# Performance work log

Hardware: AMD Instinct MI355X
Metric: run time of the kernel (lower is better)

Reference implementation:

```python
import jax, jax.numpy as jnp
import numpy as np

D_MODEL = 2048
D_INNER = 4096  # d_model * expand_factor
LN_EPS = 1e-5


def setup_inputs() -> dict:
    key = jax.random.key(0)
    k1, k2, k3, k4 = jax.random.split(key, 4)
    B, S = 2, 4096
    x = jax.random.normal(k1, (B, S, D_MODEL), dtype=jnp.float32)
    gamma = jnp.ones((D_MODEL,), dtype=jnp.float32)
    beta = jnp.zeros((D_MODEL,), dtype=jnp.float32)
    # nn.Linear-like small init to keep activations in-range
    W_in = jax.random.normal(k2, (2 * D_INNER, D_MODEL), dtype=jnp.float32) * 0.02
    W_out = jax.random.normal(k3, (D_MODEL, D_INNER), dtype=jnp.float32) * 0.02
    dt_min, dt_max = 0.001, 0.1
    dt = jax.random.uniform(k4, (D_INNER,), dtype=jnp.float32) * (dt_max - dt_min) + dt_min
    return {"x": x, "gamma": gamma, "beta": beta, "W_in": W_in, "W_out": W_out, "dt": dt}


def reference(x, gamma, beta, W_in, W_out, dt):
    # x: [B, S, D_MODEL]
    identity = x
    # LayerNorm over last dim
    mu = jnp.mean(x, axis=-1, keepdims=True)
    var = jnp.mean(jnp.square(x - mu), axis=-1, keepdims=True)
    xn = (x - mu) * jax.lax.rsqrt(var + LN_EPS) * gamma + beta
    # in_proj: [B, S, 2*D_INNER]
    projected = jnp.einsum("bsd,ed->bse", xn, W_in)
    z, gate = jnp.split(projected, 2, axis=-1)
    # z gated by sigmoid of clamped z (clamp only inside sigmoid)
    z_gated = z * jax.nn.sigmoid(jnp.clip(z, -15.0, 15.0))
    # temporal weighting by softmax(-dt) over d_inner
    dt_weights = jax.nn.softmax(-dt)  # [D_INNER]
    z_temporal = z_gated * dt_weights  # broadcast over [B, S, D_INNER]
    # gate path: silu on clamped gate
    output = z_temporal * jax.nn.silu(jnp.clip(gate, -15.0, 15.0))
    # out_proj back to d_model
    output = jnp.einsum("bse,de->bsd", output, W_out)
    return output + identity
```

## Files before the change

kernel.cpp:

```cpp
#include <hip/hip_runtime.h>
#include <cstdint>
#include <cstddef>

#define T_TOK 8192
#define DM    2048
#define DI    4096
#define TWO_DI 8192

typedef __attribute__((ext_vector_type(8))) short bf16x8;
typedef __attribute__((ext_vector_type(4))) float f32x4;

__device__ __forceinline__ unsigned short f2bf(float f) {
  union { float f; unsigned u; } c; c.f = f;
  unsigned u = c.u;
  unsigned r = (u + 0x7fffu + ((u >> 16) & 1u)) >> 16;
  return (unsigned short)r;
}

__global__ __launch_bounds__(256) void ln_kernel(
    const float* __restrict__ x, const float* __restrict__ gamma,
    const float* __restrict__ beta, unsigned short* __restrict__ xn) {
  const int t = blockIdx.x;
  const int tid = threadIdx.x;
  const float* row = x + (size_t)t * DM;
  float4 v0 = reinterpret_cast<const float4*>(row)[tid];
  float4 v1 = reinterpret_cast<const float4*>(row)[tid + 256];
  float s  = v0.x + v0.y + v0.z + v0.w + v1.x + v1.y + v1.z + v1.w;
  float ss = v0.x*v0.x + v0.y*v0.y + v0.z*v0.z + v0.w*v0.w
           + v1.x*v1.x + v1.y*v1.y + v1.z*v1.z + v1.w*v1.w;
  #pragma unroll
  for (int off = 32; off > 0; off >>= 1) {
    s  += __shfl_down(s, off);
    ss += __shfl_down(ss, off);
  }
  __shared__ float red[8];
  __shared__ float mu_s, inv_s;
  if ((tid & 63) == 0) { red[tid >> 6] = s; red[4 + (tid >> 6)] = ss; }
  __syncthreads();
  if (tid == 0) {
    float S  = red[0] + red[1] + red[2] + red[3];
    float SS = red[4] + red[5] + red[6] + red[7];
    float mu  = S * (1.0f / DM);
    float var = SS * (1.0f / DM) - mu * mu;
    mu_s = mu;
    inv_s = rsqrtf(var + 1e-5f);
  }
  __syncthreads();
  const float mu = mu_s, inv = inv_s;
  float4 g0 = reinterpret_cast<const float4*>(gamma)[tid];
  float4 b0 = reinterpret_cast<const float4*>(beta)[tid];
  float4 g1 = reinterpret_cast<const float4*>(gamma)[tid + 256];
  float4 b1 = reinterpret_cast<const float4*>(beta)[tid + 256];
  ushort4 o0, o1;
  o0.x = f2bf((v0.x - mu) * inv * g0.x + b0.x);
  o0.y = f2bf((v0.y - mu) * inv * g0.y + b0.y);
  o0.z = f2bf((v0.z - mu) * inv * g0.z + b0.z);
  o0.w = f2bf((v0.w - mu) * inv * g0.w + b0.w);
  o1.x = f2bf((v1.x - mu) * inv * g1.x + b1.x);
  o1.y = f2bf((v1.y - mu) * inv * g1.y + b1.y);
  o1.z = f2bf((v1.z - mu) * inv * g1.z + b1.z);
  o1.w = f2bf((v1.w - mu) * inv * g1.w + b1.w);
  reinterpret_cast<ushort4*>(xn + (size_t)t * DM)[tid]       = o0;
  reinterpret_cast<ushort4*>(xn + (size_t)t * DM)[tid + 256] = o1;
}

__global__ __launch_bounds__(256) void cvt_both(
    const float* __restrict__ a, unsigned short* __restrict__ oa, int n4a,
    const float* __restrict__ b, unsigned short* __restrict__ ob, int n4b) {
  int i = blockIdx.x * 256 + threadIdx.x;
  const float* src;
  unsigned short* dst;
  int idx;
  if (i < n4a) { src = a; dst = oa; idx = i; }
  else { idx = i - n4a; if (idx >= n4b) return; src = b; dst = ob; }
  float4 v = reinterpret_cast<const float4*>(src)[idx];
  ushort4 o;
  o.x = f2bf(v.x); o.y = f2bf(v.y); o.z = f2bf(v.z); o.w = f2bf(v.w);
  reinterpret_cast<ushort4*>(dst)[idx] = o;
}

__global__ __launch_bounds__(256) void dt_softmax(
    const float* __restrict__ dt, float* __restrict__ w) {
  const int tid = threadIdx.x;
  float e[16];
  float local = 0.f;
  #pragma unroll
  for (int i = 0; i < 16; ++i) {
    float v = __expf(-dt[i * 256 + tid]);
    e[i] = v;
    local += v;
  }
  #pragma unroll
  for (int off = 32; off > 0; off >>= 1) local += __shfl_down(local, off);
  __shared__ float red[4];
  __shared__ float tot;
  if ((tid & 63) == 0) red[tid >> 6] = local;
  __syncthreads();
  if (tid == 0) tot = red[0] + red[1] + red[2] + red[3];
  __syncthreads();
  const float inv = 1.f / tot;
  #pragma unroll
  for (int i = 0; i < 16; ++i) w[i * 256 + tid] = e[i] * inv;
}

__device__ __forceinline__ float actf(float z, float g, float w) {
  float zc = fminf(fmaxf(z, -15.f), 15.f);
  float sz = 1.f / (1.f + __expf(-zc));
  float gc = fminf(fmaxf(g, -15.f), 15.f);
  float sg = 1.f / (1.f + __expf(-gc));
  return z * sz * w * gc * sg;
}

#define BAR()    __builtin_amdgcn_s_barrier()
#define SCHED0() __builtin_amdgcn_sched_barrier(0)
#define PRIO1()  __builtin_amdgcn_s_setprio(1)
#define PRIO0()  __builtin_amdgcn_s_setprio(0)
#define WAIT_LGKM0() asm volatile("s_waitcnt lgkmcnt(0)" ::: "memory")
#define WAIT_VM6()   asm volatile("s_waitcnt vmcnt(6)" ::: "memory")

#define GLD16(gaddr, laddr) __builtin_amdgcn_global_load_lds(                 \
    (const __attribute__((address_space(1))) void*)(gaddr),                   \
    (__attribute__((address_space(3))) void*)(laddr), 16, 0, 0)

#define STAGE(ldsbase, gb, k0) do {                                           \
    GLD16((gb) + sOff  + (k0), &(ldsbase)[tid * 8]);                          \
    GLD16((gb) + sOff2 + (k0), &(ldsbase)[tid * 8 + 4096]);                   \
  } while (0)

#define G1_NKT 32
#define G1_NIT 16

__global__ __launch_bounds__(512, 2) void gemm1_fused8(
    const unsigned short* __restrict__ A, const unsigned short* __restrict__ W,
    const float* __restrict__ dtw, unsigned short* __restrict__ act) {
  __shared__ unsigned short lA [2][256 * 64];
  __shared__ unsigned short lB1[2][128 * 64];
  __shared__ unsigned short lB2[2][128 * 64];

  const int tid  = threadIdx.x;
  const int lane = tid & 63;
  const int wmI  = (tid >> 6) >> 2;
  const int wnI  = (tid >> 6) & 3;
  const int tM = blockIdx.y * 256;
  const int tN = blockIdx.x * 128;

  const int r0   = lane & 15;
  const int hi4  = lane >> 4;
  const int swz0 = (hi4 ^ (r0 & 7)) << 3;
  const int swz1 = swz0 ^ 32;
  const int aRow = (wmI * 128 + r0) * 64;
  const int bRow = (wnI * 32  + r0) * 64;

  const int srow = tid >> 3;
  const int scol = ((tid & 7) ^ (srow & 7)) << 3;
  const size_t sOff  = (size_t)srow * DM + scol;
  const size_t sOff2 = sOff + (size_t)64 * DM;

  const unsigned short* Ab    = A + (size_t)tM * DM;
  const unsigned short* Ab128 = Ab + (size_t)128 * DM;
  const unsigned short* B1b   = W + (size_t)tN * DM;
  const unsigned short* B2b   = W + (size_t)(tN + DI) * DM;

  f32x4 accZ[8][2], accG[8][2];
  #pragma unroll
  for (int i = 0; i < 8; ++i)
    #pragma unroll
    for (int j = 0; j < 2; ++j) {
      accZ[i][j] = f32x4{0.f, 0.f, 0.f, 0.f};
      accG[i][j] = f32x4{0.f, 0.f, 0.f, 0.f};
    }
  bf16x8 af[8][2], b1f[2][2], b2f[2][2];

#define G1_READ(b) do {                                                       \
    _Pragma("unroll") for (int i = 0; i < 8; ++i) {                           \
      af[i][0] = *reinterpret_cast<const bf16x8*>(&lA[b][aRow + i*1024 + swz0]); \
      af[i][1] = *reinterpret_cast<const bf16x8*>(&lA[b][aRow + i*1024 + swz1]); \
    }                                                                         \
    _Pragma("unroll") for (int j = 0; j < 2; ++j) {                           \
      b1f[j][0] = *reinterpret_cast<const bf16x8*>(&lB1[b][bRow + j*1024 + swz0]); \
      b1f[j][1] = *reinterpret_cast<const bf16x8*>(&lB1[b][bRow + j*1024 + swz1]); \
      b2f[j][0] = *reinterpret_cast<const bf16x8*>(&lB2[b][bRow + j*1024 + swz0]); \
      b2f[j][1] = *reinterpret_cast<const bf16x8*>(&lB2[b][bRow + j*1024 + swz1]); \
    }                                                                         \
  } while (0)

#define G1_MFMA(kh, ib) do {                                                  \
    _Pragma("unroll") for (int i = 0; i < 4; ++i)                             \
      _Pragma("unroll") for (int j = 0; j < 2; ++j) {                         \
        accZ[ib+i][j] = __builtin_amdgcn_mfma_f32_16x16x32_bf16(              \
            af[ib+i][kh], b1f[j][kh], accZ[ib+i][j], 0, 0, 0);                \
        accG[ib+i][j] = __builtin_amdgcn_mfma_f32_16x16x32_bf16(              \
            af[ib+i][kh], b2f[j][kh], accG[ib+i][j], 0, 0, 0);                \
      }                                                                       \
  } while (0)

  STAGE(lA[0],        Ab,    0);
  STAGE(&lA[0][8192], Ab128, 0);
  STAGE(lB1[0],       B1b,   0);
  STAGE(lB2[0],       B2b,   0);
  STAGE(lA[1],        Ab,    64);
  STAGE(&lA[1][8192], Ab128, 64);
  STAGE(lB1[1],       B1b,   64);
  WAIT_VM6();
  BAR();

  #pragma unroll 1
  for (int t = 0; t < G1_NIT; ++t) {
    const int k1  = (2 * t + 1) * 64;
    const int kt2 = 2 * t + 2;
    const int kt3 = 2 * t + 3;
    const int k2 = (kt2 < G1_NKT ? kt2 : G1_NKT - 1) * 64;
    const int k3 = (kt3 < G1_NKT ? kt3 : G1_NKT - 1) * 64;

    G1_READ(0);
    STAGE(lB2[1], B2b, k1);
    BAR(); WAIT_LGKM0(); SCHED0();
    PRIO1(); G1_MFMA(0, 0); PRIO0();
    SCHED0(); BAR();
    STAGE(lA[0], Ab, k2);
    BAR(); SCHED0();
    PRIO1(); G1_MFMA(0, 4); PRIO0();
    SCHED0(); BAR();
    STAGE(&lA[0][8192], Ab128, k2);
    BAR(); SCHED0();
    PRIO1(); G1_MFMA(1, 0); PRIO0();
    SCHED0(); BAR();
    STAGE(lB1[0], B1b, k2);
    WAIT_VM6();
    BAR(); SCHED0();
    PRIO1(); G1_MFMA(1, 4); PRIO0();
    SCHED0(); BAR();
    G1_READ(1);
    STAGE(lB2[0], B2b, k2);
    BAR(); WAIT_LGKM0(); SCHED0();
    PRIO1(); G1_MFMA(0, 0); PRIO0();
    SCHED0(); BAR();
    STAGE(lA[1], Ab, k3);
    BAR(); SCHED0();
    PRIO1(); G1_MFMA(0, 4); PRIO0();
    SCHED0(); BAR();
    STAGE(&lA[1][8192], Ab128, k3);
    BAR(); SCHED0();
    PRIO1(); G1_MFMA(1, 0); PRIO0();
    SCHED0(); BAR();
    STAGE(lB1[1], B1b, k3);
    WAIT_VM6();
    BAR(); SCHED0();
    PRIO1(); G1_MFMA(1, 4); PRIO0();
    SCHED0(); BAR();
  }

  const int qr   = hi4 << 2;
  const int colb = tN + wnI * 32 + r0;
  const float w0 = dtw[colb];
  const float w1 = dtw[colb + 16];
  #pragma unroll
  for (int i = 0; i < 8; ++i) {
    #pragma unroll
    for (int r = 0; r < 4; ++r) {
      const size_t base = (size_t)(tM + wmI * 128 + i * 16 + qr + r) * DI + colb;
      act[base]      = f2bf(actf(accZ[i][0][r], accG[i][0][r], w0));
      act[base + 16] = f2bf(actf(accZ[i][1][r], accG[i][1][r], w1));
    }
  }
#undef G1_READ
#undef G1_MFMA
}

#define G2_NKT 64
#define G2_NIT 32

__global__ __launch_bounds__(512, 2) void gemm2_res8(
    const unsigned short* __restrict__ A, const unsigned short* __restrict__ Bm,
    float* __restrict__ out, const float* __restrict__ ident) {
  __shared__ unsigned short lA[2][256 * 64];
  __shared__ unsigned short lB[2][256 * 64];

  const int tid  = threadIdx.x;
  const int lane = tid & 63;
  const int wmI  = (tid >> 6) >> 2;
  const int wnI  = (tid >> 6) & 3;
  const int tM = blockIdx.y * 256;
  const int tN = blockIdx.x * 256;

  const int r0   = lane & 15;
  const int hi4  = lane >> 4;
  const int swz0 = (hi4 ^ (r0 & 7)) << 3;
  const int swz1 = swz0 ^ 32;
  const int aRow = (wmI * 128 + r0) * 64;
  const int bRow = (wnI * 64  + r0) * 64;

  const int srow = tid >> 3;
  const int scol = ((tid & 7) ^ (srow & 7)) << 3;
  const size_t sOff  = (size_t)srow * DI + scol;
  const size_t sOff2 = sOff + (size_t)64 * DI;

  const unsigned short* Ab    = A + (size_t)tM * DI;
  const unsigned short* Ab128 = Ab + (size_t)128 * DI;
  const unsigned short* Bb    = Bm + (size_t)tN * DI;
  const unsigned short* Bb128 = Bb + (size_t)128 * DI;

  f32x4 acc[8][4];
  #pragma unroll
  for (int i = 0; i < 8; ++i)
    #pragma unroll
    for (int j = 0; j < 4; ++j) acc[i][j] = f32x4{0.f, 0.f, 0.f, 0.f};
  bf16x8 af[8][2], bfr[4][2];

#define G2_READ(b) do {                                                       \
    _Pragma("unroll") for (int i = 0; i < 8; ++i) {                           \
      af[i][0] = *reinterpret_cast<const bf16x8*>(&lA[b][aRow + i*1024 + swz0]); \
      af[i][1] = *reinterpret_cast<const bf16x8*>(&lA[b][aRow + i*1024 + swz1]); \
    }                                                                         \
    _Pragma("unroll") for (int j = 0; j < 4; ++j) {                           \
      bfr[j][0] = *reinterpret_cast<const bf16x8*>(&lB[b][bRow + j*1024 + swz0]); \
      bfr[j][1] = *reinterpret_cast<const bf16x8*>(&lB[b][bRow + j*1024 + swz1]); \
    }                                                                         \
  } while (0)

#define G2_MFMA(kh, ib) do {                                                  \
    _Pragma("unroll") for (int i = 0; i < 4; ++i)                             \
      _Pragma("unroll") for (int j = 0; j < 4; ++j)                           \
        acc[ib+i][j] = __builtin_amdgcn_mfma_f32_16x16x32_bf16(               \
            af[ib+i][kh], bfr[j][kh], acc[ib+i][j], 0, 0, 0);                 \
  } while (0)

  STAGE(lA[0],        Ab,    0);
  STAGE(&lA[0][8192], Ab128, 0);
  STAGE(lB[0],        Bb,    0);
  STAGE(&lB[0][8192], Bb128, 0);
  STAGE(lA[1],        Ab,    64);
  STAGE(&lA[1][8192], Ab128, 64);
  STAGE(lB[1],        Bb,    64);
  WAIT_VM6();
  BAR();

  #pragma unroll 1
  for (int t = 0; t < G2_NIT; ++t) {
    const int k1  = (2 * t + 1) * 64;
    const int kt2 = 2 * t + 2;
    const int kt3 = 2 * t + 3;
    const int k2 = (kt2 < G2_NKT ? kt2 : G2_NKT - 1) * 64;
    const int k3 = (kt3 < G2_NKT ? kt3 : G2_NKT - 1) * 64;

    G2_READ(0);
    STAGE(&lB[1][8192], Bb128, k1);
    BAR(); WAIT_LGKM0(); SCHED0();
    PRIO1(); G2_MFMA(0, 0); PRIO0();
    SCHED0(); BAR();
    STAGE(lA[0], Ab, k2);
    BAR(); SCHED0();
    PRIO1(); G2_MFMA(0, 4); PRIO0();
    SCHED0(); BAR();
    STAGE(&lA[0][8192], Ab128, k2);
    BAR(); SCHED0();
    PRIO1(); G2_MFMA(1, 0); PRIO0();
    SCHED0(); BAR();
    STAGE(lB[0], Bb, k2);
    WAIT_VM6();
    BAR(); SCHED0();
    PRIO1(); G2_MFMA(1, 4); PRIO0();
    SCHED0(); BAR();
    G2_READ(1);
    STAGE(&lB[0][8192], Bb128, k2);
    BAR(); WAIT_LGKM0(); SCHED0();
    PRIO1(); G2_MFMA(0, 0); PRIO0();
    SCHED0(); BAR();
    STAGE(lA[1], Ab, k3);
    BAR(); SCHED0();
    PRIO1(); G2_MFMA(0, 4); PRIO0();
    SCHED0(); BAR();
    STAGE(&lA[1][8192], Ab128, k3);
    BAR(); SCHED0();
    PRIO1(); G2_MFMA(1, 0); PRIO0();
    SCHED0(); BAR();
    STAGE(lB[1], Bb, k3);
    WAIT_VM6();
    BAR(); SCHED0();
    PRIO1(); G2_MFMA(1, 4); PRIO0();
    SCHED0(); BAR();
  }

  const int qr   = hi4 << 2;
  const int colb = tN + wnI * 64 + r0;
  #pragma unroll
  for (int i = 0; i < 8; ++i) {
    #pragma unroll
    for (int r = 0; r < 4; ++r) {
      const size_t rowoff = (size_t)(tM + wmI * 128 + i * 16 + qr + r) * DM;
      #pragma unroll
      for (int j = 0; j < 4; ++j) {
        const size_t idx = rowoff + colb + j * 16;
        out[idx] = acc[i][j][r] + ident[idx];
      }
    }
  }
#undef G2_READ
#undef G2_MFMA
}

extern "C" void kernel_launch(void* const* d_in, const int* in_sizes, int n_in,
                              void* d_out, int out_size, void* d_ws, size_t ws_size,
                              hipStream_t stream) {
  const float* x     = (const float*)d_in[0];
  const float* gamma = (const float*)d_in[1];
  const float* beta  = (const float*)d_in[2];
  const float* W_in  = (const float*)d_in[3];
  const float* W_out = (const float*)d_in[4];
  const float* dt    = (const float*)d_in[5];
  float* out = (float*)d_out;

  char* ws = (char*)d_ws;
  unsigned short* xn     = (unsigned short*)(ws);
  unsigned short* win_b  = (unsigned short*)(ws + ((size_t)32 << 20));
  unsigned short* wout_b = (unsigned short*)(ws + ((size_t)64 << 20));
  float*          dtw    = (float*)(ws + ((size_t)80 << 20));
  unsigned short* act    = (unsigned short*)(ws + ((size_t)96 << 20));

  const int n4_in  = TWO_DI * DM / 4;
  const int n4_out = DM * DI / 4;

  ln_kernel<<<T_TOK, 256, 0, stream>>>(x, gamma, beta, xn);
  cvt_both<<<(n4_in + n4_out + 255) / 256, 256, 0, stream>>>(
      W_in, win_b, n4_in, W_out, wout_b, n4_out);
  dt_softmax<<<1, 256, 0, stream>>>(dt, dtw);

  gemm1_fused8<<<dim3(DI / 128, T_TOK / 256), 512, 0, stream>>>(
      xn, win_b, dtw, act);

  gemm2_res8<<<dim3(DM / 256, T_TOK / 256), 512, 0, stream>>>(
      act, wout_b, out, x);
}
```

Baseline: 599.4 us.

## Interleave LDS fragment loads with MFMA phases and restage double-buffer prefetch order

Both GEMM kernels stop loading all A/B fragments for a full K-tile into registers up front. They now load small register sets (4 A and 2 or 4 B fragments) right before each group of 16 MFMAs, which lowers register pressure. The global-to-LDS prefetch schedule is reordered to issue A-halves and B-halves in pairs, with the vmcnt wait changed from 6 to 4. This risks more LDS round-trip stalls between MFMA phases, because each phase now waits on its own lgkm loads.

Measured after the change: 574.5 us. 1.04x faster.

```diff
diff --git a/kernel.cpp b/kernel.cpp
--- a/kernel.cpp
+++ b/kernel.cpp
@@ -116,7 +116,7 @@
 #define PRIO1()  __builtin_amdgcn_s_setprio(1)
 #define PRIO0()  __builtin_amdgcn_s_setprio(0)
 #define WAIT_LGKM0() asm volatile("s_waitcnt lgkmcnt(0)" ::: "memory")
-#define WAIT_VM6()   asm volatile("s_waitcnt vmcnt(6)" ::: "memory")
+#define WAIT_VM4()   asm volatile("s_waitcnt vmcnt(4)" ::: "memory")
 
 #define GLD16(gaddr, laddr) __builtin_amdgcn_global_load_lds(                 \
     (const __attribute__((address_space(1))) void*)(gaddr),                   \
@@ -169,39 +169,42 @@
       accZ[i][j] = f32x4{0.f, 0.f, 0.f, 0.f};
       accG[i][j] = f32x4{0.f, 0.f, 0.f, 0.f};
     }
-  bf16x8 af[8][2], b1f[2][2], b2f[2][2];
-
-#define G1_READ(b) do {                                                       \
-    _Pragma("unroll") for (int i = 0; i < 8; ++i) {                           \
-      af[i][0] = *reinterpret_cast<const bf16x8*>(&lA[b][aRow + i*1024 + swz0]); \
-      af[i][1] = *reinterpret_cast<const bf16x8*>(&lA[b][aRow + i*1024 + swz1]); \
+  bf16x8 aR[4], bR1[2], bR2[2];
+
+#define G1_LDA(b, idx, sw) do {                                               \
+    _Pragma("unroll") for (int i = 0; i < 4; ++i)                             \
+      aR[i] = *reinterpret_cast<const bf16x8*>(                               \
+          &lA[b][aRow + ((idx) + i) * 1024 + (sw)]);                          \
+  } while (0)
+#define G1_LDB(b, sw) do {                                                    \
+    _Pragma("unroll") for (int j = 0; j < 2; ++j) {                           \
+      bR1[j] = *reinterpret_cast<const bf16x8*>(&lB1[b][bRow + j*1024 + (sw)]); \
+      bR2[j] = *reinterpret_cast<const bf16x8*>(&lB2[b][bRow + j*1024 + (sw)]); \
     }                                                                         \
-    _Pragma("unroll") for (int j = 0; j < 2; ++j) {                           \
-      b1f[j][0] = *reinterpret_cast<const bf16x8*>(&lB1[b][bRow + j*1024 + swz0]); \
-      b1f[j][1] = *reinterpret_cast<const bf16x8*>(&lB1[b][bRow + j*1024 + swz1]); \
-      b2f[j][0] = *reinterpret_cast<const bf16x8*>(&lB2[b][bRow + j*1024 + swz0]); \
-      b2f[j][1] = *reinterpret_cast<const bf16x8*>(&lB2[b][bRow + j*1024 + swz1]); \
-    }                                                                         \
-  } while (0)
-
-#define G1_MFMA(kh, ib) do {                                                  \
+  } while (0)
+#define G1_MFMA16(ib) do {                                                    \
     _Pragma("unroll") for (int i = 0; i < 4; ++i)                             \
       _Pragma("unroll") for (int j = 0; j < 2; ++j) {                         \
-        accZ[ib+i][j] = __builtin_amdgcn_mfma_f32_16x16x32_bf16(              \
-            af[ib+i][kh], b1f[j][kh], accZ[ib+i][j], 0, 0, 0);                \
-        accG[ib+i][j] = __builtin_amdgcn_mfma_f32_16x16x32_bf16(              \
-            af[ib+i][kh], b2f[j][kh], accG[ib+i][j], 0, 0, 0);                \
+        accZ[(ib)+i][j] = __builtin_amdgcn_mfma_f32_16x16x32_bf16(            \
+            aR[i], bR1[j], accZ[(ib)+i][j], 0, 0, 0);                         \
+        accG[(ib)+i][j] = __builtin_amdgcn_mfma_f32_16x16x32_bf16(            \
+            aR[i], bR2[j], accG[(ib)+i][j], 0, 0, 0);                         \
       }                                                                       \
+  } while (0)
+#define G1_TAIL() do {                                                        \
+    BAR(); WAIT_LGKM0(); SCHED0();                                            \
+  } while (0)
+#define G1_MF(ib) do {                                                        \
+    PRIO1(); G1_MFMA16(ib); PRIO0(); SCHED0(); BAR();                         \
   } while (0)
 
   STAGE(lA[0],        Ab,    0);
   STAGE(&lA[0][8192], Ab128, 0);
   STAGE(lB1[0],       B1b,   0);
   STAGE(lB2[0],       B2b,   0);
-  STAGE(lA[1],        Ab,    64);
-  STAGE(&lA[1][8192], Ab128, 64);
   STAGE(lB1[1],       B1b,   64);
-  WAIT_VM6();
+  STAGE(lB2[1],       B2b,   64);
+  WAIT_VM4();
   BAR();
 
   #pragma unroll 1
@@ -212,42 +215,29 @@
     const int k2 = (kt2 < G1_NKT ? kt2 : G1_NKT - 1) * 64;
     const int k3 = (kt3 < G1_NKT ? kt3 : G1_NKT - 1) * 64;
 
-    G1_READ(0);
-    STAGE(lB2[1], B2b, k1);
-    BAR(); WAIT_LGKM0(); SCHED0();
-    PRIO1(); G1_MFMA(0, 0); PRIO0();
-    SCHED0(); BAR();
-    STAGE(lA[0], Ab, k2);
-    BAR(); SCHED0();
-    PRIO1(); G1_MFMA(0, 4); PRIO0();
-    SCHED0(); BAR();
-    STAGE(&lA[0][8192], Ab128, k2);
-    BAR(); SCHED0();
-    PRIO1(); G1_MFMA(1, 0); PRIO0();
-    SCHED0(); BAR();
-    STAGE(lB1[0], B1b, k2);
-    WAIT_VM6();
-    BAR(); SCHED0();
-    PRIO1(); G1_MFMA(1, 4); PRIO0();
-    SCHED0(); BAR();
-    G1_READ(1);
-    STAGE(lB2[0], B2b, k2);
-    BAR(); WAIT_LGKM0(); SCHED0();
-    PRIO1(); G1_MFMA(0, 0); PRIO0();
-    SCHED0(); BAR();
-    STAGE(lA[1], Ab, k3);
-    BAR(); SCHED0();
-    PRIO1(); G1_MFMA(0, 4); PRIO0();
-    SCHED0(); BAR();
-    STAGE(&lA[1][8192], Ab128, k3);
-    BAR(); SCHED0();
-    PRIO1(); G1_MFMA(1, 0); PRIO0();
-    SCHED0(); BAR();
-    STAGE(lB1[1], B1b, k3);
-    WAIT_VM6();
-    BAR(); SCHED0();
-    PRIO1(); G1_MFMA(1, 4); PRIO0();
-    SCHED0(); BAR();
+    G1_LDA(0, 0, swz0); G1_LDB(0, swz0);
+    STAGE(lA[1], Ab, k1); STAGE(&lA[1][8192], Ab128, k1);
+    G1_TAIL(); G1_MF(0);
+    G1_LDA(0, 4, swz0);
+    G1_TAIL(); G1_MF(4);
+    G1_LDA(0, 0, swz1); G1_LDB(0, swz1);
+    G1_TAIL(); G1_MF(0);
+    G1_LDA(0, 4, swz1);
+    STAGE(lB1[0], B1b, k2); STAGE(lB2[0], B2b, k2);
+    WAIT_VM4();
+    G1_TAIL(); G1_MF(4);
+
+    G1_LDA(1, 0, swz0); G1_LDB(1, swz0);
+    STAGE(lA[0], Ab, k2); STAGE(&lA[0][8192], Ab128, k2);
+    G1_TAIL(); G1_MF(0);
+    G1_LDA(1, 4, swz0);
+    G1_TAIL(); G1_MF(4);
+    G1_LDA(1, 0, swz1); G1_LDB(1, swz1);
+    G1_TAIL(); G1_MF(0);
+    G1_LDA(1, 4, swz1);
+    STAGE(lB1[1], B1b, k3); STAGE(lB2[1], B2b, k3);
+    WAIT_VM4();
+    G1_TAIL(); G1_MF(4);
   }
 
   const int qr   = hi4 << 2;
@@ -263,8 +253,11 @@
       act[base + 16] = f2bf(actf(accZ[i][1][r], accG[i][1][r], w1));
     }
   }
-#undef G1_READ
-#undef G1_MFMA
+#undef G1_LDA
+#undef G1_LDB
+#undef G1_MFMA16
+#undef G1_TAIL
+#undef G1_MF
 }
 
 #define G2_NKT 64
@@ -305,34 +298,37 @@
   for (int i = 0; i < 8; ++i)
     #pragma unroll
     for (int j = 0; j < 4; ++j) acc[i][j] = f32x4{0.f, 0.f, 0.f, 0.f};
-  bf16x8 af[8][2], bfr[4][2];
-
-#define G2_READ(b) do {                                                       \
-    _Pragma("unroll") for (int i = 0; i < 8; ++i) {                           \
-      af[i][0] = *reinterpret_cast<const bf16x8*>(&lA[b][aRow + i*1024 + swz0]); \
-      af[i][1] = *reinterpret_cast<const bf16x8*>(&lA[b][aRow + i*1024 + swz1]); \
-    }                                                                         \
-    _Pragma("unroll") for (int j = 0; j < 4; ++j) {                           \
-      bfr[j][0] = *reinterpret_cast<const bf16x8*>(&lB[b][bRow + j*1024 + swz0]); \
-      bfr[j][1] = *reinterpret_cast<const bf16x8*>(&lB[b][bRow + j*1024 + swz1]); \
-    }                                                                         \
-  } while (0)
-
-#define G2_MFMA(kh, ib) do {                                                  \
+  bf16x8 aR[4], bR[4];
+
+#define G2_LDA(b, idx, sw) do {                                               \
+    _Pragma("unroll") for (int i = 0; i < 4; ++i)                             \
+      aR[i] = *reinterpret_cast<const bf16x8*>(                               \
+          &lA[b][aRow + ((idx) + i) * 1024 + (sw)]);                          \
+  } while (0)
+#define G2_LDB(b, sw) do {                                                    \
+    _Pragma("unroll") for (int j = 0; j < 4; ++j)                             \
+      bR[j] = *reinterpret_cast<const bf16x8*>(&lB[b][bRow + j*1024 + (sw)]); \
+  } while (0)
+#define G2_MFMA16(ib) do {                                                    \
     _Pragma("unroll") for (int i = 0; i < 4; ++i)                             \
       _Pragma("unroll") for (int j = 0; j < 4; ++j)                           \
-        acc[ib+i][j] = __builtin_amdgcn_mfma_f32_16x16x32_bf16(               \
-            af[ib+i][kh], bfr[j][kh], acc[ib+i][j], 0, 0, 0);                 \
+        acc[(ib)+i][j] = __builtin_amdgcn_mfma_f32_16x16x32_bf16(             \
+            aR[i], bR[j], acc[(ib)+i][j], 0, 0, 0);                           \
+  } while (0)
+#define G2_TAIL() do {                                                        \
+    BAR(); WAIT_LGKM0(); SCHED0();                                            \
+  } while (0)
+#define G2_MF(ib) do {                                                        \
+    PRIO1(); G2_MFMA16(ib); PRIO0(); SCHED0(); BAR();                         \
   } while (0)
 
   STAGE(lA[0],        Ab,    0);
   STAGE(&lA[0][8192], Ab128, 0);
   STAGE(lB[0],        Bb,    0);
   STAGE(&lB[0][8192], Bb128, 0);
-  STAGE(lA[1],        Ab,    64);
-  STAGE(&lA[1][8192], Ab128, 64);
   STAGE(lB[1],        Bb,    64);
-  WAIT_VM6();
+  STAGE(&lB[1][8192], Bb128, 64);
+  WAIT_VM4();
   BAR();
 
   #pragma unroll 1
@@ -343,42 +339,29 @@
     const int k2 = (kt2 < G2_NKT ? kt2 : G2_NKT - 1) * 64;
     const int k3 = (kt3 < G2_NKT ? kt3 : G2_NKT - 1) * 64;
 
-    G2_READ(0);
-    STAGE(&lB[1][8192], Bb128, k1);
-    BAR(); WAIT_LGKM0(); SCHED0();
-    PRIO1(); G2_MFMA(0, 0); PRIO0();
-    SCHED0(); BAR();
-    STAGE(lA[0], Ab, k2);
-    BAR(); SCHED0();
-    PRIO1(); G2_MFMA(0, 4); PRIO0();
-    SCHED0(); BAR();
-    STAGE(&lA[0][8192], Ab128, k2);
-    BAR(); SCHED0();
-    PRIO1(); G2_MFMA(1, 0); PRIO0();
-    SCHED0(); BAR();
-    STAGE(lB[0], Bb, k2);
-    WAIT_VM6();
-    BAR(); SCHED0();
-    PRIO1(); G2_MFMA(1, 4); PRIO0();
-    SCHED0(); BAR();
-    G2_READ(1);
-    STAGE(&lB[0][8192], Bb128, k2);
-    BAR(); WAIT_LGKM0(); SCHED0();
-    PRIO1(); G2_MFMA(0, 0); PRIO0();
-    SCHED0(); BAR();
-    STAGE(lA[1], Ab, k3);
-    BAR(); SCHED0();
-    PRIO1(); G2_MFMA(0, 4); PRIO0();
-    SCHED0(); BAR();
-    STAGE(&lA[1][8192], Ab128, k3);
-    BAR(); SCHED0();
-    PRIO1(); G2_MFMA(1, 0); PRIO0();
-    SCHED0(); BAR();
-    STAGE(lB[1], Bb, k3);
-    WAIT_VM6();
-    BAR(); SCHED0();
-    PRIO1(); G2_MFMA(1, 4); PRIO0();
-    SCHED0(); BAR();
+    G2_LDA(0, 0, swz0); G2_LDB(0, swz0);
+    STAGE(lA[1], Ab, k1); STAGE(&lA[1][8192], Ab128, k1);
+    G2_TAIL(); G2_MF(0);
+    G2_LDA(0, 4, swz0);
+    G2_TAIL(); G2_MF(4);
+    G2_LDA(0, 0, swz1); G2_LDB(0, swz1);
+    G2_TAIL(); G2_MF(0);
+    G2_LDA(0, 4, swz1);
+    STAGE(lB[0], Bb, k2); STAGE(&lB[0][8192], Bb128, k2);
+    WAIT_VM4();
+    G2_TAIL(); G2_MF(4);
+
+    G2_LDA(1, 0, swz0); G2_LDB(1, swz0);
+    STAGE(lA[0], Ab, k2); STAGE(&lA[0][8192], Ab128, k2);
+    G2_TAIL(); G2_MF(0);
+    G2_LDA(1, 4, swz0);
+    G2_TAIL(); G2_MF(4);
+    G2_LDA(1, 0, swz1); G2_LDB(1, swz1);
+    G2_TAIL(); G2_MF(0);
+    G2_LDA(1, 4, swz1);
+    STAGE(lB[1], Bb, k3); STAGE(&lB[1][8192], Bb128, k3);
+    WAIT_VM4();
+    G2_TAIL(); G2_MF(4);
   }
 
   const int qr   = hi4 << 2;
@@ -395,8 +378,11 @@
       }
     }
   }
-#undef G2_READ
-#undef G2_MFMA
+#undef G2_LDA
+#undef G2_LDB
+#undef G2_MFMA16
+#undef G2_TAIL
+#undef G2_MF
 }
 
 extern "C" void kernel_launch(void* const* d_in, const int* in_sizes, int n_in,
```

## Split GEMM tiles into quadrant-wise LDS reads interleaved with staged loads

Applied to the files above, without the earlier changes.

Both GEMM kernels now split each warp's output into quadrants. The A fragments come from the two 128-row halves of LDS and the B fragments from two halves. Each quadrant's LDS fragment reads are issued just before its MFMA block, overlapping with the next global-to-LDS stage. The goal is a smaller per-phase register footprint and better overlap of LDS reads with MFMA work. In exchange the wave-to-row/column mapping changes (the epilogue indexing was updated to match), and there are more LDS waits and barriers per iteration.

New measurement: 586.9 us. 2.1% less time.

```diff
diff --git a/kernel.cpp b/kernel.cpp
--- a/kernel.cpp
+++ b/kernel.cpp
@@ -127,6 +127,8 @@
     GLD16((gb) + sOff2 + (k0), &(ldsbase)[tid * 8 + 4096]);                   \
   } while (0)
 
+#define TAIL() do { BAR(); WAIT_LGKM0(); SCHED0(); } while (0)
+
 #define G1_NKT 32
 #define G1_NIT 16
 
@@ -148,8 +150,8 @@
   const int hi4  = lane >> 4;
   const int swz0 = (hi4 ^ (r0 & 7)) << 3;
   const int swz1 = swz0 ^ 32;
-  const int aRow = (wmI * 128 + r0) * 64;
-  const int bRow = (wnI * 32  + r0) * 64;
+  const int aRow0 = (wmI * 64 + r0) * 64;
+  const int bRow  = (wnI * 32 + r0) * 64;
 
   const int srow = tid >> 3;
   const int scol = ((tid & 7) ^ (srow & 7)) << 3;
@@ -169,38 +171,45 @@
       accZ[i][j] = f32x4{0.f, 0.f, 0.f, 0.f};
       accG[i][j] = f32x4{0.f, 0.f, 0.f, 0.f};
     }
-  bf16x8 af[8][2], b1f[2][2], b2f[2][2];
-
-#define G1_READ(b) do {                                                       \
-    _Pragma("unroll") for (int i = 0; i < 8; ++i) {                           \
-      af[i][0] = *reinterpret_cast<const bf16x8*>(&lA[b][aRow + i*1024 + swz0]); \
-      af[i][1] = *reinterpret_cast<const bf16x8*>(&lA[b][aRow + i*1024 + swz1]); \
-    }                                                                         \
+  bf16x8 a0[4][2], a1[4][2], bz[2][2], bg[2][2];
+
+#define G1_LDA0(b) do {                                                       \
+    _Pragma("unroll") for (int i = 0; i < 4; ++i) {                           \
+      a0[i][0] = *reinterpret_cast<const bf16x8*>(&lA[b][aRow0 + i*1024 + swz0]); \
+      a0[i][1] = *reinterpret_cast<const bf16x8*>(&lA[b][aRow0 + i*1024 + swz1]); \
+    } } while (0)
+#define G1_LDA1(b) do {                                                       \
+    _Pragma("unroll") for (int i = 0; i < 4; ++i) {                           \
+      a1[i][0] = *reinterpret_cast<const bf16x8*>(&lA[b][8192 + aRow0 + i*1024 + swz0]); \
+      a1[i][1] = *reinterpret_cast<const bf16x8*>(&lA[b][8192 + aRow0 + i*1024 + swz1]); \
+    } } while (0)
+#define G1_LDBZ(b) do {                                                       \
     _Pragma("unroll") for (int j = 0; j < 2; ++j) {                           \
-      b1f[j][0] = *reinterpret_cast<const bf16x8*>(&lB1[b][bRow + j*1024 + swz0]); \
-      b1f[j][1] = *reinterpret_cast<const bf16x8*>(&lB1[b][bRow + j*1024 + swz1]); \
-      b2f[j][0] = *reinterpret_cast<const bf16x8*>(&lB2[b][bRow + j*1024 + swz0]); \
-      b2f[j][1] = *reinterpret_cast<const bf16x8*>(&lB2[b][bRow + j*1024 + swz1]); \
-    }                                                                         \
+      bz[j][0] = *reinterpret_cast<const bf16x8*>(&lB1[b][bRow + j*1024 + swz0]); \
+      bz[j][1] = *reinterpret_cast<const bf16x8*>(&lB1[b][bRow + j*1024 + swz1]); \
+    } } while (0)
+#define G1_LDBG(b) do {                                                       \
+    _Pragma("unroll") for (int j = 0; j < 2; ++j) {                           \
+      bg[j][0] = *reinterpret_cast<const bf16x8*>(&lB2[b][bRow + j*1024 + swz0]); \
+      bg[j][1] = *reinterpret_cast<const bf16x8*>(&lB2[b][bRow + j*1024 + swz1]); \
+    } } while (0)
+#define G1_Q(accA, ioff, af) do {                                             \
+    PRIO1();                                                                  \
+    _Pragma("unroll") for (int kh = 0; kh < 2; ++kh)                          \
+      _Pragma("unroll") for (int i = 0; i < 4; ++i)                           \
+        _Pragma("unroll") for (int j = 0; j < 2; ++j)                         \
+          accA[(ioff)+i][j] = __builtin_amdgcn_mfma_f32_16x16x32_bf16(        \
+              af[i][kh], G1_BF[j][kh], accA[(ioff)+i][j], 0, 0, 0);           \
+    PRIO0(); SCHED0(); BAR();                                                 \
   } while (0)
 
-#define G1_MFMA(kh, ib) do {                                                  \
-    _Pragma("unroll") for (int i = 0; i < 4; ++i)                             \
-      _Pragma("unroll") for (int j = 0; j < 2; ++j) {                         \
-        accZ[ib+i][j] = __builtin_amdgcn_mfma_f32_16x16x32_bf16(              \
-            af[ib+i][kh], b1f[j][kh], accZ[ib+i][j], 0, 0, 0);                \
-        accG[ib+i][j] = __builtin_amdgcn_mfma_f32_16x16x32_bf16(              \
-            af[ib+i][kh], b2f[j][kh], accG[ib+i][j], 0, 0, 0);                \
-      }                                                                       \
-  } while (0)
-
   STAGE(lA[0],        Ab,    0);
-  STAGE(&lA[0][8192], Ab128, 0);
   STAGE(lB1[0],       B1b,   0);
   STAGE(lB2[0],       B2b,   0);
+  STAGE(&lA[0][8192], Ab128, 0);
   STAGE(lA[1],        Ab,    64);
-  STAGE(&lA[1][8192], Ab128, 64);
   STAGE(lB1[1],       B1b,   64);
+  STAGE(lB2[1],       B2b,   64);
   WAIT_VM6();
   BAR();
 
@@ -212,42 +221,43 @@
     const int k2 = (kt2 < G1_NKT ? kt2 : G1_NKT - 1) * 64;
     const int k3 = (kt3 < G1_NKT ? kt3 : G1_NKT - 1) * 64;
 
-    G1_READ(0);
-    STAGE(lB2[1], B2b, k1);
-    BAR(); WAIT_LGKM0(); SCHED0();
-    PRIO1(); G1_MFMA(0, 0); PRIO0();
-    SCHED0(); BAR();
+#define G1_BF bz
+    G1_LDA0(0); G1_LDBZ(0);
+    STAGE(&lA[1][8192], Ab128, k1);
+    TAIL(); G1_Q(accZ, 0, a0);
+#undef G1_BF
+#define G1_BF bg
+    G1_LDBG(0);
     STAGE(lA[0], Ab, k2);
-    BAR(); SCHED0();
-    PRIO1(); G1_MFMA(0, 4); PRIO0();
-    SCHED0(); BAR();
+    TAIL(); G1_Q(accG, 0, a0);
+    G1_LDA1(0);
+    STAGE(lB1[0], B1b, k2);
+    TAIL(); G1_Q(accG, 4, a1);
+#undef G1_BF
+#define G1_BF bz
+    STAGE(lB2[0], B2b, k2);
+    WAIT_VM6();
+    TAIL(); G1_Q(accZ, 4, a1);
+#undef G1_BF
+
+#define G1_BF bz
+    G1_LDA0(1); G1_LDBZ(1);
     STAGE(&lA[0][8192], Ab128, k2);
-    BAR(); SCHED0();
-    PRIO1(); G1_MFMA(1, 0); PRIO0();
-    SCHED0(); BAR();
-    STAGE(lB1[0], B1b, k2);
+    TAIL(); G1_Q(accZ, 0, a0);
+#undef G1_BF
+#define G1_BF bg
+    G1_LDBG(1);
+    STAGE(lA[1], Ab, k3);
+    TAIL(); G1_Q(accG, 0, a0);
+    G1_LDA1(1);
+    STAGE(lB1[1], B1b, k3);
+    TAIL(); G1_Q(accG, 4, a1);
+#undef G1_BF
+#define G1_BF bz
+    STAGE(lB2[1], B2b, k3);
     WAIT_VM6();
-    BAR(); SCHED0();
-    PRIO1(); G1_MFMA(1, 4); PRIO0();
-    SCHED0(); BAR();
-    G1_READ(1);
-    STAGE(lB2[0], B2b, k2);
-    BAR(); WAIT_LGKM0(); SCHED0();
-    PRIO1(); G1_MFMA(0, 0); PRIO0();
-    SCHED0(); BAR();
-    STAGE(lA[1], Ab, k3);
-    BAR(); SCHED0();
-    PRIO1(); G1_MFMA(0, 4); PRIO0();
-    SCHED0(); BAR();
-    STAGE(&lA[1][8192], Ab128, k3);
-    BAR(); SCHED0();
-    PRIO1(); G1_MFMA(1, 0); PRIO0();
-    SCHED0(); BAR();
-    STAGE(lB1[1], B1b, k3);
-    WAIT_VM6();
-    BAR(); SCHED0();
-    PRIO1(); G1_MFMA(1, 4); PRIO0();
-    SCHED0(); BAR();
+    TAIL(); G1_Q(accZ, 4, a1);
+#undef G1_BF
   }
 
   const int qr   = hi4 << 2;
@@ -256,15 +266,19 @@
   const float w1 = dtw[colb + 16];
   #pragma unroll
   for (int i = 0; i < 8; ++i) {
+    const int rowb = tM + wmI * 64 + ((i & 3) << 4) + ((i >> 2) << 7) + qr;
     #pragma unroll
     for (int r = 0; r < 4; ++r) {
-      const size_t base = (size_t)(tM + wmI * 128 + i * 16 + qr + r) * DI + colb;
+      const size_t base = (size_t)(rowb + r) * DI + colb;
       act[base]      = f2bf(actf(accZ[i][0][r], accG[i][0][r], w0));
       act[base + 16] = f2bf(actf(accZ[i][1][r], accG[i][1][r], w1));
     }
   }
-#undef G1_READ
-#undef G1_MFMA
+#undef G1_LDA0
+#undef G1_LDA1
+#undef G1_LDBZ
+#undef G1_LDBG
+#undef G1_Q
 }
 
 #define G2_NKT 64
@@ -287,8 +301,8 @@
   const int hi4  = lane >> 4;
   const int swz0 = (hi4 ^ (r0 & 7)) << 3;
   const int swz1 = swz0 ^ 32;
-  const int aRow = (wmI * 128 + r0) * 64;
-  const int bRow = (wnI * 64  + r0) * 64;
+  const int aRow0 = (wmI * 64 + r0) * 64;
+  const int bRow  = (wnI * 32 + r0) * 64;
 
   const int srow = tid >> 3;
   const int scol = ((tid & 7) ^ (srow & 7)) << 3;
@@ -305,33 +319,45 @@
   for (int i = 0; i < 8; ++i)
     #pragma unroll
     for (int j = 0; j < 4; ++j) acc[i][j] = f32x4{0.f, 0.f, 0.f, 0.f};
-  bf16x8 af[8][2], bfr[4][2];
-
-#define G2_READ(b) do {                                                       \
-    _Pragma("unroll") for (int i = 0; i < 8; ++i) {                           \
-      af[i][0] = *reinterpret_cast<const bf16x8*>(&lA[b][aRow + i*1024 + swz0]); \
-      af[i][1] = *reinterpret_cast<const bf16x8*>(&lA[b][aRow + i*1024 + swz1]); \
-    }                                                                         \
-    _Pragma("unroll") for (int j = 0; j < 4; ++j) {                           \
-      bfr[j][0] = *reinterpret_cast<const bf16x8*>(&lB[b][bRow + j*1024 + swz0]); \
-      bfr[j][1] = *reinterpret_cast<const bf16x8*>(&lB[b][bRow + j*1024 + swz1]); \
-    }                                                                         \
+  bf16x8 a0[4][2], a1[4][2], b0[2][2], b1[2][2];
+
+#define G2_LDA0(b) do {                                                       \
+    _Pragma("unroll") for (int i = 0; i < 4; ++i) {                           \
+      a0[i][0] = *reinterpret_cast<const bf16x8*>(&lA[b][aRow0 + i*1024 + swz0]); \
+      a0[i][1] = *reinterpret_cast<const bf16x8*>(&lA[b][aRow0 + i*1024 + swz1]); \
+    } } while (0)
+#define G2_LDA1(b) do {                                                       \
+    _Pragma("unroll") for (int i = 0; i < 4; ++i) {                           \
+      a1[i][0] = *reinterpret_cast<const bf16x8*>(&lA[b][8192 + aRow0 + i*1024 + swz0]); \
+      a1[i][1] = *reinterpret_cast<const bf16x8*>(&lA[b][8192 + aRow0 + i*1024 + swz1]); \
+    } } while (0)
+#define G2_LDB0(b) do {                                                       \
+    _Pragma("unroll") for (int j = 0; j < 2; ++j) {                           \
+      b0[j][0] = *reinterpret_cast<const bf16x8*>(&lB[b][bRow + j*1024 + swz0]); \
+      b0[j][1] = *reinterpret_cast<const bf16x8*>(&lB[b][bRow + j*1024 + swz1]); \
+    } } while (0)
+#define G2_LDB1(b) do {                                                       \
+    _Pragma("unroll") for (int j = 0; j < 2; ++j) {                           \
+      b1[j][0] = *reinterpret_cast<const bf16x8*>(&lB[b][8192 + bRow + j*1024 + swz0]); \
+      b1[j][1] = *reinterpret_cast<const bf16x8*>(&lB[b][8192 + bRow + j*1024 + swz1]); \
+    } } while (0)
+#define G2_Q(ioff, joff, af, bf) do {                                         \
+    PRIO1();                                                                  \
+    _Pragma("unroll") for (int kh = 0; kh < 2; ++kh)                          \
+      _Pragma("unroll") for (int i = 0; i < 4; ++i)                           \
+        _Pragma("unroll") for (int j = 0; j < 2; ++j)                         \
+          acc[(ioff)+i][(joff)+j] = __builtin_amdgcn_mfma_f32_16x16x32_bf16(  \
+              af[i][kh], bf[j][kh], acc[(ioff)+i][(joff)+j], 0, 0, 0);        \
+    PRIO0(); SCHED0(); BAR();                                                 \
   } while (0)
 
-#define G2_MFMA(kh, ib) do {                                                  \
-    _Pragma("unroll") for (int i = 0; i < 4; ++i)                             \
-      _Pragma("unroll") for (int j = 0; j < 4; ++j)                           \
-        acc[ib+i][j] = __builtin_amdgcn_mfma_f32_16x16x32_bf16(               \
-            af[ib+i][kh], bfr[j][kh], acc[ib+i][j], 0, 0, 0);                 \
-  } while (0)
-
   STAGE(lA[0],        Ab,    0);
-  STAGE(&lA[0][8192], Ab128, 0);
   STAGE(lB[0],        Bb,    0);
   STAGE(&lB[0][8192], Bb128, 0);
+  STAGE(&lA[0][8192], Ab128, 0);
   STAGE(lA[1],        Ab,    64);
-  STAGE(&lA[1][8192], Ab128, 64);
   STAGE(lB[1],        Bb,    64);
+  STAGE(&lB[1][8192], Bb128, 64);
   WAIT_VM6();
   BAR();
 
@@ -343,60 +369,53 @@
     const int k2 = (kt2 < G2_NKT ? kt2 : G2_NKT - 1) * 64;
     const int k3 = (kt3 < G2_NKT ? kt3 : G2_NKT - 1) * 64;
 
-    G2_READ(0);
-    STAGE(&lB[1][8192], Bb128, k1);
-    BAR(); WAIT_LGKM0(); SCHED0();
-    PRIO1(); G2_MFMA(0, 0); PRIO0();
-    SCHED0(); BAR();
+    G2_LDA0(0); G2_LDB0(0);
+    STAGE(&lA[1][8192], Ab128, k1);
+    TAIL(); G2_Q(0, 0, a0, b0);
+    G2_LDB1(0);
     STAGE(lA[0], Ab, k2);
-    BAR(); SCHED0();
-    PRIO1(); G2_MFMA(0, 4); PRIO0();
-    SCHED0(); BAR();
+    TAIL(); G2_Q(0, 2, a0, b1);
+    G2_LDA1(0);
+    STAGE(lB[0], Bb, k2);
+    TAIL(); G2_Q(4, 2, a1, b1);
+    STAGE(&lB[0][8192], Bb128, k2);
+    WAIT_VM6();
+    TAIL(); G2_Q(4, 0, a1, b0);
+
+    G2_LDA0(1); G2_LDB0(1);
     STAGE(&lA[0][8192], Ab128, k2);
-    BAR(); SCHED0();
-    PRIO1(); G2_MFMA(1, 0); PRIO0();
-    SCHED0(); BAR();
-    STAGE(lB[0], Bb, k2);
+    TAIL(); G2_Q(0, 0, a0, b0);
+    G2_LDB1(1);
+    STAGE(lA[1], Ab, k3);
+    TAIL(); G2_Q(0, 2, a0, b1);
+    G2_LDA1(1);
+    STAGE(lB[1], Bb, k3);
+    TAIL(); G2_Q(4, 2, a1, b1);
+    STAGE(&lB[1][8192], Bb128, k3);
     WAIT_VM6();
-    BAR(); SCHED0();
-    PRIO1(); G2_MFMA(1, 4); PRIO0();
-    SCHED0(); BAR();
-    G2_READ(1);
-    STAGE(&lB[0][8192], Bb128, k2);
-    BAR(); WAIT_LGKM0(); SCHED0();
-    PRIO1(); G2_MFMA(0, 0); PRIO0();
-    SCHED0(); BAR();
-    STAGE(lA[1], Ab, k3);
-    BAR(); SCHED0();
-    PRIO1(); G2_MFMA(0, 4); PRIO0();
-    SCHED0(); BAR();
-    STAGE(&lA[1][8192], Ab128, k3);
-    BAR(); SCHED0();
-    PRIO1(); G2_MFMA(1, 0); PRIO0();
-    SCHED0(); BAR();
-    STAGE(lB[1], Bb, k3);
-    WAIT_VM6();
-    BAR(); SCHED0();
-    PRIO1(); G2_MFMA(1, 4); PRIO0();
-    SCHED0(); BAR();
+    TAIL(); G2_Q(4, 0, a1, b0);
   }
 
   const int qr   = hi4 << 2;
-  const int colb = tN + wnI * 64 + r0;
+  const int colb = tN + wnI * 32 + r0;
   #pragma unroll
   for (int i = 0; i < 8; ++i) {
+    const int rowb = tM + wmI * 64 + ((i & 3) << 4) + ((i >> 2) << 7) + qr;
     #pragma unroll
     for (int r = 0; r < 4; ++r) {
-      const size_t rowoff = (size_t)(tM + wmI * 128 + i * 16 + qr + r) * DM;
+      const size_t rowoff = (size_t)(rowb + r) * DM;
       #pragma unroll
       for (int j = 0; j < 4; ++j) {
-        const size_t idx = rowoff + colb + j * 16;
+        const size_t idx = rowoff + colb + ((j & 1) << 4) + ((j >> 1) << 7);
         out[idx] = acc[i][j][r] + ident[idx];
       }
     }
   }
-#undef G2_READ
-#undef G2_MFMA
+#undef G2_LDA0
+#undef G2_LDA1
+#undef G2_LDB0
+#undef G2_LDB1
+#undef G2_Q
 }
 
 extern "C" void kernel_launch(void* const* d_in, const int* in_sizes, int n_in,
```
